# Performance work log

Hardware: AMD Instinct MI355X
Metric: run time of the kernel (lower is better)

The kernel has to match this reference:

```python
import jax, jax.numpy as jnp
import numpy as np

ALPHA = 0.2      # LeakyReLU negative slope
NEG_INF = -9e15  # mask value from the original code

def setup_inputs() -> dict:
    key = jax.random.key(0)
    k1, k2, k3, k4 = jax.random.split(key, 4)
    B, M, F_IN, F_OUT = 16, 2048, 128, 64
    h = jax.random.normal(k1, (B, M, F_IN), dtype=jnp.float32)
    adj = jax.random.randint(k2, (B, M, M), 0, 2, dtype=jnp.int32)
    W = jax.random.normal(k3, (F_IN, F_OUT), dtype=jnp.float32) * 0.1
    a = jax.random.normal(k4, (2 * F_OUT, 1), dtype=jnp.float32) * 0.1
    return {"h": h, "adj": adj, "W": W, "a": a}

def reference(h, adj, W, a):
    # h: [B,M,Fin], adj: [B,M,M], W: [Fin,E], a: [2E,1]
    Wh = jnp.matmul(h, W)                      # [B,M,E]
    E = Wh.shape[-1]
    a1, a2 = a[:E, 0], a[E:, 0]
    # decompose a^T [Wh_i || Wh_j] = (Wh_i . a1) + (Wh_j . a2)
    f1 = Wh @ a1                               # [B,M] (source/query term)
    f2 = Wh @ a2                               # [B,M] (target/key term)
    e = jax.nn.leaky_relu(f1[:, :, None] + f2[:, None, :], negative_slope=ALPHA)  # [B,M,M]
    scores = jnp.where(adj > 0, e, NEG_INF)
    attn = jax.nn.softmax(scores, axis=-1)     # [B,M,M]  (dropout p=0 / eval mode)
    h_prime = jnp.matmul(attn, Wh)             # [B,M,E]
    return jax.nn.elu(h_prime)                 # concat=True branch
```

## Files before the change

kernel.cpp:

```cpp
#include <hip/hip_runtime.h>


#define M_     2048
#define FIN_   128
#define F_     64
#define ALPHA_ 0.2f

typedef float  float4_ __attribute__((ext_vector_type(4)));
typedef short  short4_ __attribute__((ext_vector_type(4)));
typedef short  short8  __attribute__((ext_vector_type(8)));
typedef int    int4_   __attribute__((ext_vector_type(4)));
typedef unsigned short u16;
typedef unsigned int   u32;

static __device__ __forceinline__ float bf2f(u16 u) {
    return __uint_as_float(((u32)u) << 16);
}
static __device__ __forceinline__ u16 f2bf(float f) {
    u32 u = __float_as_uint(f);
    u32 r = u + 0x7FFFu + ((u >> 16) & 1u);
    return (u16)(r >> 16);
}


__global__ __launch_bounds__(256) void k_pre(
    const float* __restrict__ h, const float* __restrict__ W,
    const float* __restrict__ a, u16* __restrict__ WhT,
    float* __restrict__ f1, float* __restrict__ f2)
{
    const int row = blockIdx.x * 4 + (threadIdx.x >> 6);
    const int n   = threadIdx.x & 63;

    float acc = 0.f;
    const float* hp = h + (size_t)row * FIN_;
#pragma unroll 8
    for (int k = 0; k < FIN_; ++k)
        acc += hp[k] * W[k * F_ + n];

    const int b = row >> 11, jm = row & 2047;
    WhT[((size_t)b * F_ + n) * M_ + jm] = f2bf(acc);

    float s1 = acc * a[n], s2 = acc * a[F_ + n];
#pragma unroll
    for (int off = 1; off < 64; off <<= 1) {
        s1 += __shfl_xor(s1, off, 64);
        s2 += __shfl_xor(s2, off, 64);
    }
    if (n == 0) { f1[row] = s1; f2[row] = s2; }
}

__global__ __launch_bounds__(256, 4) void k_attn2(
    const int* __restrict__ adj, const u16* __restrict__ WhT,
    const float* __restrict__ f1, const float* __restrict__ f2,
    float* __restrict__ out)
{
    __shared__ float f2s[M_];
    __shared__ float f1s[32];
    __shared__ float dens[32];

    const int tid  = threadIdx.x;
    const int w    = tid >> 6;
    const int l    = tid & 63;
    const int lc   = l & 15;
    const int quad = l >> 4;
    const int b    = blockIdx.x >> 6;
    const int i0   = (blockIdx.x & 63) * 32;
    const int mt   = w & 1;
    const int ntp  = w >> 1;

    {
        const float4_* src = (const float4_*)(f2 + b * M_);
        float4_* dst = (float4_*)f2s;
        for (int i = tid; i < M_ / 4; i += 256) dst[i] = src[i];
    }
    if (tid < 32) f1s[tid] = f1[b * M_ + i0 + tid];
    __syncthreads();

    const float f1r = f1s[mt * 16 + lc];
    const int*  ap  = adj + ((size_t)(b * M_ + i0 + mt * 16 + lc)) * M_ + quad * 8;
    const u16*  wp0 = WhT + (size_t)b * F_ * M_ + (size_t)(ntp * 32 + lc) * M_ + quad * 8;
    const u16*  wp1 = wp0 + (size_t)16 * M_;
    const float* fp = f2s + quad * 8;

    float4_ acc0 = (float4_){0.f, 0.f, 0.f, 0.f};
    float4_ acc1 = (float4_){0.f, 0.f, 0.f, 0.f};
    float dsum = 0.f;

#pragma unroll 4
    for (int it = 0; it < 64; ++it) {
        const int j0 = it * 32;
        int4_   c0 = *(const int4_*)(ap + j0);
        int4_   c1 = *(const int4_*)(ap + j0 + 4);
        short8  b0 = *(const short8*)(wp0 + j0);
        short8  b1 = *(const short8*)(wp1 + j0);
        float4_ g0 = *(const float4_*)(fp + j0);
        float4_ g1 = *(const float4_*)(fp + j0 + 4);

        short8 af;
        float d = 0.f;
#define GAT_SC(jj, ai, gi)                                          \
        {                                                           \
            float x_ = f1r + (gi);                                  \
            x_ = fmaxf(x_, ALPHA_ * x_);                            \
            float e_ = ((ai) > 0) ? __expf(x_) : 0.f;               \
            u16 pb_ = f2bf(e_);                                     \
            af[jj] = (short)pb_;                                    \
            d += bf2f(pb_);                                         \
        }
        GAT_SC(0, c0[0], g0[0]) GAT_SC(1, c0[1], g0[1])
        GAT_SC(2, c0[2], g0[2]) GAT_SC(3, c0[3], g0[3])
        GAT_SC(4, c1[0], g1[0]) GAT_SC(5, c1[1], g1[1])
        GAT_SC(6, c1[2], g1[2]) GAT_SC(7, c1[3], g1[3])
#undef GAT_SC
        dsum += d;

        acc0 = __builtin_amdgcn_mfma_f32_16x16x32_bf16(af, b0, acc0, 0, 0, 0);
        acc1 = __builtin_amdgcn_mfma_f32_16x16x32_bf16(af, b1, acc1, 0, 0, 0);
    }

    dsum += __shfl_xor(dsum, 16, 64);
    dsum += __shfl_xor(dsum, 32, 64);
    if (w < 2 && l < 16) dens[mt * 16 + l] = dsum;
    __syncthreads();

#pragma unroll
    for (int mm = 0; mm < 4; ++mm) {
        const int rr  = mt * 16 + quad * 4 + mm;
        const float den  = dens[rr];
        const float rden = (den > 0.f) ? (1.f / den) : 0.f;
        float* op = out + ((size_t)(b * M_ + i0 + rr)) * F_ + ntp * 32 + lc;
        float v0 = acc0[mm] * rden;
        float v1 = acc1[mm] * rden;
        op[0]  = v0 > 0.f ? v0 : expm1f(v0);
        op[16] = v1 > 0.f ? v1 : expm1f(v1);
    }
}

#define ROWS_  32
#define TS_    36
#define WT_    132

__global__ __launch_bounds__(256, 4) void k_gat2(
    const float* __restrict__ h, const int* __restrict__ adj,
    const float* __restrict__ W, const float* __restrict__ a,
    float* __restrict__ out)
{
    __shared__ u16   Wl[FIN_ * F_];
    __shared__ float a_s[2 * F_];
    __shared__ float wa1[FIN_], wa2[FIN_];
    __shared__ float f1s[ROWS_];
    __shared__ float dens[ROWS_];
    __shared__ char  dyn[32 * WT_ * 4];

    u16*   hT   = (u16*)dyn;
    u16*   P    = (u16*)(dyn + 9216);
    float* f2t  = (float*)(dyn + 11520);
    float* Tsum = (float*)dyn;

    const int tid  = threadIdx.x;
    const int w    = tid >> 6;
    const int l    = tid & 63;
    const int lc   = l & 15;
    const int quad = l >> 4;
    const int b    = blockIdx.x >> 6;
    const int i0   = (blockIdx.x & 63) * ROWS_;

    if (tid < 128) a_s[tid] = a[tid];
    for (int e = tid; e < FIN_ * F_; e += 256) Wl[e] = f2bf(W[e]);
    __syncthreads();

    if (tid < FIN_) {
        float s1 = 0.f, s2 = 0.f;
#pragma unroll 8
        for (int n = 0; n < F_; ++n) {
            float wv = W[tid * F_ + n];
            s1 += wv * a_s[n];
            s2 += wv * a_s[F_ + n];
        }
        wa1[tid] = s1;
        wa2[tid] = s2;
    }
    __syncthreads();

    {
        const int i = tid >> 3, sub = tid & 7, k0 = sub * 16;
        const float* hp = h + ((size_t)(b * M_ + i0 + i)) * FIN_ + k0;
        float s = 0.f;
#pragma unroll
        for (int k = 0; k < 16; ++k) s += hp[k] * wa1[k0 + k];
        s += __shfl_xor(s, 1, 64);
        s += __shfl_xor(s, 2, 64);
        s += __shfl_xor(s, 4, 64);
        if (sub == 0) f1s[i] = s;
    }
    __syncthreads();

    const int prow = tid >> 3;
    const int ps   = tid & 7;
    const int sf0  = (tid & 15) * 8;
    const int stp  = (tid >> 4) * 2;
    const int mt   = w & 1;
    const int ntb  = (w >> 1) * 4;
    const float f1r = f1s[prow];
    float denacc = 0.f;

    float4_ acc[4];
#pragma unroll
    for (int c = 0; c < 4; ++c) acc[c] = (float4_){0.f, 0.f, 0.f, 0.f};

    const int*   aprow = adj + ((size_t)(b * M_ + i0 + prow)) * M_ + ps * 4;
    const float* hbase = h + ((size_t)(b * M_ + stp)) * FIN_ + sf0;

    for (int it = 0; it < 64; ++it) {
        const int j0 = it * 32;
        int4_ c4 = *(const int4_*)(aprow + j0);
        {
            const float* hp0 = hbase + (size_t)j0 * FIN_;
            const float* hp1 = hp0 + FIN_;
            float4_ x0 = *(const float4_*)hp0, x1 = *(const float4_*)(hp0 + 4);
            float4_ y0 = *(const float4_*)hp1, y1 = *(const float4_*)(hp1 + 4);
            float xa[8] = {x0[0], x0[1], x0[2], x0[3], x1[0], x1[1], x1[2], x1[3]};
            float ya[8] = {y0[0], y0[1], y0[2], y0[3], y1[0], y1[1], y1[2], y1[3]};
            float fp0 = 0.f, fp1 = 0.f;
#pragma unroll
            for (int kk = 0; kk < 8; ++kk) {
                const int k = sf0 + kk;
                u16 u0 = f2bf(xa[kk]), u1 = f2bf(ya[kk]);
                *(u32*)(hT + k * TS_ + stp) = (u32)u0 | ((u32)u1 << 16);
                fp0 += xa[kk] * wa2[k];
                fp1 += ya[kk] * wa2[k];
            }
            fp0 += __shfl_xor(fp0, 1, 64); fp1 += __shfl_xor(fp1, 1, 64);
            fp0 += __shfl_xor(fp0, 2, 64); fp1 += __shfl_xor(fp1, 2, 64);
            fp0 += __shfl_xor(fp0, 4, 64); fp1 += __shfl_xor(fp1, 4, 64);
            fp0 += __shfl_xor(fp0, 8, 64); fp1 += __shfl_xor(fp1, 8, 64);
            if ((tid & 15) == 0) { f2t[stp] = fp0; f2t[stp + 1] = fp1; }
        }
        __syncthreads();
        {
            float4_ g = *(const float4_*)(f2t + ps * 4);
            u32 pk0, pk1;
            float d = 0.f;
            {
                float x_ = f1r + g[0]; x_ = fmaxf(x_, ALPHA_ * x_);
                float e_ = (c4[0] > 0) ? __expf(x_) : 0.f;
                u16 pb = f2bf(e_); d += bf2f(pb); pk0 = (u32)pb;
            }
            {
                float x_ = f1r + g[1]; x_ = fmaxf(x_, ALPHA_ * x_);
                float e_ = (c4[1] > 0) ? __expf(x_) : 0.f;
                u16 pb = f2bf(e_); d += bf2f(pb); pk0 |= ((u32)pb << 16);
            }
            {
                float x_ = f1r + g[2]; x_ = fmaxf(x_, ALPHA_ * x_);
                float e_ = (c4[2] > 0) ? __expf(x_) : 0.f;
                u16 pb = f2bf(e_); d += bf2f(pb); pk1 = (u32)pb;
            }
            {
                float x_ = f1r + g[3]; x_ = fmaxf(x_, ALPHA_ * x_);
                float e_ = (c4[3] > 0) ? __expf(x_) : 0.f;
                u16 pb = f2bf(e_); d += bf2f(pb); pk1 |= ((u32)pb << 16);
            }
            *(u32*)(P + prow * TS_ + ps * 4)     = pk0;
            *(u32*)(P + prow * TS_ + ps * 4 + 2) = pk1;
            denacc += d;
        }
        __syncthreads();
        {
            const u16* apx = P + (mt * 16 + lc) * TS_ + quad * 8;
            short4_ a0 = *(const short4_*)apx;
            short4_ a1 = *(const short4_*)(apx + 4);
            short8 af;
            af[0] = a0[0]; af[1] = a0[1]; af[2] = a0[2]; af[3] = a0[3];
            af[4] = a1[0]; af[5] = a1[1]; af[6] = a1[2]; af[7] = a1[3];
#pragma unroll
            for (int c = 0; c < 4; ++c) {
                const u16* bp = hT + ((ntb + c) * 16 + lc) * TS_ + quad * 8;
                short4_ b0 = *(const short4_*)bp;
                short4_ b1 = *(const short4_*)(bp + 4);
                short8 bf;
                bf[0] = b0[0]; bf[1] = b0[1]; bf[2] = b0[2]; bf[3] = b0[3];
                bf[4] = b1[0]; bf[5] = b1[1]; bf[6] = b1[2]; bf[7] = b1[3];
                acc[c] = __builtin_amdgcn_mfma_f32_16x16x32_bf16(af, bf, acc[c], 0, 0, 0);
            }
        }
        __syncthreads();
    }

    denacc += __shfl_xor(denacc, 1, 64);
    denacc += __shfl_xor(denacc, 2, 64);
    denacc += __shfl_xor(denacc, 4, 64);
    if (ps == 0) dens[prow] = denacc;

#pragma unroll
    for (int c = 0; c < 4; ++c)
#pragma unroll
        for (int mm = 0; mm < 4; ++mm)
            Tsum[(mt * 16 + quad * 4 + mm) * WT_ + (ntb + c) * 16 + lc] = acc[c][mm];
    __syncthreads();

    {
        const int row = tid >> 3;
        const int n0  = (tid & 7) * 8;
        const float den  = dens[row];
        const float rden = (den > 0.f) ? (1.f / den) : 0.f;
        float u[8];
#pragma unroll
        for (int nn = 0; nn < 8; ++nn) u[nn] = 0.f;
        for (int k = 0; k < FIN_; ++k) {
            const float tv = Tsum[row * WT_ + k];
            const u16* wq = &Wl[k * F_ + n0];
#pragma unroll
            for (int nn = 0; nn < 8; ++nn) u[nn] += tv * bf2f(wq[nn]);
        }
        float4_ o0, o1;
#pragma unroll
        for (int nn = 0; nn < 8; ++nn) {
            float hv = u[nn] * rden;
            float o  = hv > 0.f ? hv : expm1f(hv);
            if (nn < 4) o0[nn] = o; else o1[nn - 4] = o;
        }
        float* op = out + ((size_t)(b * M_ + i0 + row)) * F_ + n0;
        *(float4_*)op       = o0;
        *(float4_*)(op + 4) = o1;
    }
}

extern "C" void kernel_launch(void* const* d_in, const int* in_sizes, int n_in,
                              void* d_out, int out_size, void* d_ws, size_t ws_size,
                              hipStream_t stream)
{
    (void)out_size;
    const float* h  = (const float*)d_in[0];
    const int* adjp = (const int*)d_in[1];
    const float* Wp = (const float*)d_in[2];
    const float* ap = (const float*)d_in[3];
    for (int i = 0; i < n_in; ++i) {
        long s = in_sizes[i];
        if      (s == 4194304L)  h    = (const float*)d_in[i];
        else if (s == 67108864L) adjp = (const int*)d_in[i];
        else if (s == 8192L)     Wp   = (const float*)d_in[i];
        else if (s == 128L)      ap   = (const float*)d_in[i];
    }
    float* out = (float*)d_out;

    const size_t NEED = 4194304u + 131072u + 131072u;
    if (d_ws != nullptr && ws_size >= NEED) {
        char* ws = (char*)d_ws;
        u16*   WhT = (u16*)ws;
        float* f1  = (float*)(ws + 4194304);
        float* f2  = (float*)(ws + 4194304 + 131072);
        k_pre  <<<8192, 256, 0, stream>>>(h, Wp, ap, WhT, f1, f2);
        k_attn2<<<1024, 256, 0, stream>>>(adjp, WhT, f1, f2, out);
    } else {
        k_gat2<<<1024, 256, 0, stream>>>(h, adjp, Wp, ap, out);
    }
}
```

Measured before the change: 493.9 us.

## Split attention key range across warps and register-block the projection kernel

The attention kernel doubles its block to 512 threads and gives each half of the warps half of the key range. Partial accumulators and softmax denominators are combined through shared memory, and the output is written with vectorized float4 stores. This is meant to raise the number of warps in flight that stream the large int32 adjacency matrix. The projection kernel now stages W in shared memory, computes four rows per warp and packs the bf16 WhT store, cutting redundant global loads of W. The cost is extra shared memory and a block-wide reduction step.

```diff
diff --git a/kernel.cpp b/kernel.cpp
--- a/kernel.cpp
+++ b/kernel.cpp
@@ -23,40 +23,64 @@
 }
 
 
-__global__ __launch_bounds__(256) void k_pre(
+__global__ __launch_bounds__(256) void k_pre2(
     const float* __restrict__ h, const float* __restrict__ W,
     const float* __restrict__ a, u16* __restrict__ WhT,
     float* __restrict__ f1, float* __restrict__ f2)
 {
-    const int row = blockIdx.x * 4 + (threadIdx.x >> 6);
-    const int n   = threadIdx.x & 63;
-
-    float acc = 0.f;
-    const float* hp = h + (size_t)row * FIN_;
+    __shared__ float Wl[FIN_ * F_];
+    __shared__ float a_s[2 * F_];
+
+    const int tid = threadIdx.x;
+    const int w   = tid >> 6;
+    const int n   = tid & 63;
+
+    for (int e = tid; e < FIN_ * F_; e += 256) Wl[e] = W[e];
+    if (tid < 128) a_s[tid] = a[tid];
+    __syncthreads();
+
+    const int row0 = blockIdx.x * 16 + w * 4;
+    const float* hp = h + (size_t)row0 * FIN_;
+
+    float acc[4] = {0.f, 0.f, 0.f, 0.f};
 #pragma unroll 8
-    for (int k = 0; k < FIN_; ++k)
-        acc += hp[k] * W[k * F_ + n];
-
-    const int b = row >> 11, jm = row & 2047;
-    WhT[((size_t)b * F_ + n) * M_ + jm] = f2bf(acc);
-
-    float s1 = acc * a[n], s2 = acc * a[F_ + n];
-#pragma unroll
-    for (int off = 1; off < 64; off <<= 1) {
-        s1 += __shfl_xor(s1, off, 64);
-        s2 += __shfl_xor(s2, off, 64);
-    }
-    if (n == 0) { f1[row] = s1; f2[row] = s2; }
-}
-
-__global__ __launch_bounds__(256, 4) void k_attn2(
+    for (int k = 0; k < FIN_; ++k) {
+        const float wv = Wl[k * F_ + n];
+        acc[0] += hp[k] * wv;
+        acc[1] += hp[FIN_ + k] * wv;
+        acc[2] += hp[2 * FIN_ + k] * wv;
+        acc[3] += hp[3 * FIN_ + k] * wv;
+    }
+
+    const int b = row0 >> 11, jm = row0 & 2047;
+    {
+        short4_ pk;
+#pragma unroll
+        for (int r = 0; r < 4; ++r) pk[r] = (short)f2bf(acc[r]);
+        *(short4_*)(WhT + ((size_t)b * F_ + n) * M_ + jm) = pk;
+    }
+
+#pragma unroll
+    for (int r = 0; r < 4; ++r) {
+        float s1 = acc[r] * a_s[n], s2 = acc[r] * a_s[F_ + n];
+#pragma unroll
+        for (int off = 1; off < 64; off <<= 1) {
+            s1 += __shfl_xor(s1, off, 64);
+            s2 += __shfl_xor(s2, off, 64);
+        }
+        if (n == 0) { f1[row0 + r] = s1; f2[row0 + r] = s2; }
+    }
+}
+
+__global__ __launch_bounds__(512, 8) void k_attn3(
     const int* __restrict__ adj, const u16* __restrict__ WhT,
     const float* __restrict__ f1, const float* __restrict__ f2,
     float* __restrict__ out)
 {
     __shared__ float f2s[M_];
     __shared__ float f1s[32];
-    __shared__ float dens[32];
+    __shared__ float accT[2][32][66];
+    __shared__ float dens2[2][32];
 
     const int tid  = threadIdx.x;
     const int w    = tid >> 6;
@@ -66,12 +90,13 @@
     const int b    = blockIdx.x >> 6;
     const int i0   = (blockIdx.x & 63) * 32;
     const int mt   = w & 1;
-    const int ntp  = w >> 1;
+    const int ntp  = (w >> 1) & 1;
+    const int jh   = w >> 2;
 
     {
         const float4_* src = (const float4_*)(f2 + b * M_);
         float4_* dst = (float4_*)f2s;
-        for (int i = tid; i < M_ / 4; i += 256) dst[i] = src[i];
+        for (int i = tid; i < M_ / 4; i += 512) dst[i] = src[i];
     }
     if (tid < 32) f1s[tid] = f1[b * M_ + i0 + tid];
     __syncthreads();
@@ -86,8 +111,9 @@
     float4_ acc1 = (float4_){0.f, 0.f, 0.f, 0.f};
     float dsum = 0.f;
 
-#pragma unroll 4
-    for (int it = 0; it < 64; ++it) {
+    const int itEnd = jh * 32 + 32;
+#pragma unroll 2
+    for (int it = jh * 32; it < itEnd; ++it) {
         const int j0 = it * 32;
         int4_   c0 = *(const int4_*)(ap + j0);
         int4_   c1 = *(const int4_*)(ap + j0 + 4);
@@ -120,19 +146,28 @@
 
     dsum += __shfl_xor(dsum, 16, 64);
     dsum += __shfl_xor(dsum, 32, 64);
-    if (w < 2 && l < 16) dens[mt * 16 + l] = dsum;
-    __syncthreads();
+    if (ntp == 0 && l < 16) dens2[jh][mt * 16 + l] = dsum;
 
 #pragma unroll
     for (int mm = 0; mm < 4; ++mm) {
-        const int rr  = mt * 16 + quad * 4 + mm;
-        const float den  = dens[rr];
+        const int rr = mt * 16 + quad * 4 + mm;
+        accT[jh][rr][ntp * 32 + lc]      = acc0[mm];
+        accT[jh][rr][ntp * 32 + 16 + lc] = acc1[mm];
+    }
+    __syncthreads();
+
+    {
+        const int row = tid >> 4;
+        const int n0  = (tid & 15) * 4;
+        const float den  = dens2[0][row] + dens2[1][row];
         const float rden = (den > 0.f) ? (1.f / den) : 0.f;
-        float* op = out + ((size_t)(b * M_ + i0 + rr)) * F_ + ntp * 32 + lc;
-        float v0 = acc0[mm] * rden;
-        float v1 = acc1[mm] * rden;
-        op[0]  = v0 > 0.f ? v0 : expm1f(v0);
-        op[16] = v1 > 0.f ? v1 : expm1f(v1);
+        float4_ o;
+#pragma unroll
+        for (int c = 0; c < 4; ++c) {
+            float v = (accT[0][row][n0 + c] + accT[1][row][n0 + c]) * rden;
+            o[c] = v > 0.f ? v : expm1f(v);
+        }
+        *(float4_*)(out + ((size_t)(b * M_ + i0 + row)) * F_ + n0) = o;
     }
 }
 
@@ -350,8 +385,8 @@
         u16*   WhT = (u16*)ws;
         float* f1  = (float*)(ws + 4194304);
         float* f2  = (float*)(ws + 4194304 + 131072);
-        k_pre  <<<8192, 256, 0, stream>>>(h, Wp, ap, WhT, f1, f2);
-        k_attn2<<<1024, 256, 0, stream>>>(adjp, WhT, f1, f2, out);
+        k_pre2 <<<2048, 256, 0, stream>>>(h, Wp, ap, WhT, f1, f2);
+        k_attn3<<<1024, 512, 0, stream>>>(adjp, WhT, f1, f2, out);
     } else {
         k_gat2<<<1024, 256, 0, stream>>>(h, adjp, Wp, ap, out);
     }
```

Measured after the change: 466.0 us. 1.06x faster.
